# Optimization experiments

Measured on AMD Instinct MI355X. Metric: run time of the kernel, lower is better.

## Reference

```python
import jax, jax.numpy as jnp
import numpy as np
import math

B, T, M, C = 4, 2048, 16, 256   # batch, seq, m chunks, c_s chunk width
DIM = 1024                       # layer width; k = DIM // C = 4
D = 64                           # conditioning bottleneck
N_ITERS, TAU = 20, 1.0


def _diag_bias(rows, cols):
    b = np.full((rows, cols), -8.0, dtype=np.float32)
    for i in range(min(rows, cols)):
        b[i, i] = 0.0
    return jnp.asarray(b)


def setup_inputs() -> dict:
    key = jax.random.key(0)
    ks = jax.random.split(key, 10)
    state_dim = M * C
    k = DIM // C
    H_post = np.full((M, k), -8.0, dtype=np.float32)
    for i in range(M):
        H_post[i, i % k] = 0.0
    return {
        "s": jax.random.normal(ks[0], (B, T, M, C), jnp.float32),
        "gamma": 0.02 * jax.random.normal(ks[1], (state_dim,), jnp.float32),
        "compress": 0.02 * jax.random.normal(ks[2], (state_dim, D), jnp.float32),
        "alpha_pre": jnp.float32(0.01),
        "to_logits_pre": 0.02 * jax.random.normal(ks[3], (D, k * M), jnp.float32),
        "H_pre": _diag_bias(k, M),
        "alpha_align": jnp.float32(0.01),
        "to_logits_align": 0.02 * jax.random.normal(ks[4], (D, M * M), jnp.float32),
        "H_align": _diag_bias(M, M),
        "alpha_next": jnp.float32(0.01),
        "to_logits_next": 0.02 * jax.random.normal(ks[5], (D, M * M), jnp.float32),
        "H_next": _diag_bias(M, M),
        "alpha_post": jnp.float32(0.01),
        "to_logits_post": 0.02 * jax.random.normal(ks[6], (D, M * k), jnp.float32),
        "H_post": jnp.asarray(H_post),
        "W_layer": jax.random.normal(ks[7], (DIM, DIM), jnp.float32) / math.sqrt(DIM),
    }


def sinkhorn_log(logits, num_iters=N_ITERS, tau=TAU):
    """Log-domain Sinkhorn; output row-scaled so row sums = 1 * rows-normalized."""
    rows, cols = logits.shape[-2], logits.shape[-1]
    Z = logits / tau
    lr = -math.log(rows)
    lc = -math.log(cols)
    u0 = jnp.zeros(Z.shape[:-1], Z.dtype)
    v0 = jnp.zeros(Z.shape[:-2] + (cols,), Z.dtype)

    def body(_, uv):
        u, v = uv
        u = lr - jax.nn.logsumexp(Z + v[..., None, :], axis=-1)
        v = lc - jax.nn.logsumexp(Z + u[..., None], axis=-2)
        return (u, v)

    u, v = jax.lax.fori_loop(0, num_iters, body, (u0, v0))
    return jnp.exp(Z + u[..., None] + v[..., None, :]) * rows


def _route(code, alpha, to_logits, bias, state, rows, cols):
    """Fused: Sinkhorn(alpha*(code@to_logits)+bias) @ state."""
    raw = (code @ to_logits).reshape(code.shape[:-1] + (rows, cols))
    P = sinkhorn_log(alpha * raw + bias)
    return jnp.einsum('...ij,...jc->...ic', P, state)


def reference(s, gamma, compress, alpha_pre, to_logits_pre, H_pre,
              alpha_align, to_logits_align, H_align,
              alpha_next, to_logits_next, H_next,
              alpha_post, to_logits_post, H_post, W_layer):
    b, t, m, c = s.shape
    state_dim = m * c
    k = W_layer.shape[0] // c
    # RMSNorm over flattened state: F.normalize * sqrt(dim) * (gamma + 1)
    s_vec = s.reshape(b, t, state_dim)
    l2 = jnp.sqrt(jnp.sum(s_vec * s_vec, axis=-1, keepdims=True))
    s_norm = s_vec / jnp.maximum(l2, 1e-12) * jnp.sqrt(jnp.float32(state_dim)) * (gamma + 1.0)
    code = s_norm @ compress  # (b, t, d)
    # read: H_pre (k x m) routes state -> layer input
    layer_in = _route(code, alpha_pre, to_logits_pre, H_pre, s, k, m).reshape(b, t, k * c)
    layer_out = layer_in @ W_layer  # the wrapped layer_fn (dense linear)
    # write: align, absorb output via H_post, prepare next via H_next
    s_aligned = _route(code, alpha_align, to_logits_align, H_align, s, m, m)
    out_flat = layer_out.reshape(b, t, k, c)
    s_updated = s_aligned + _route(code, alpha_post, to_logits_post, H_post, out_flat, m, k)
    s_next = _route(code, alpha_next, to_logits_next, H_next, s_updated, m, m)
    return s_next
```

## Files before the change

### kernel.cpp

```cpp
#include <hip/hip_runtime.h>
#include <math.h>

#define NTOK 8192
#define SD   4096
#define ITERS 20

typedef __attribute__((ext_vector_type(8))) short short8;
typedef __attribute__((ext_vector_type(8))) unsigned short ushort8;
typedef __attribute__((ext_vector_type(4))) unsigned short us4;
typedef __attribute__((ext_vector_type(4))) float f32x4;

__device__ inline unsigned short f2bf(float x) {
    unsigned int u = __float_as_uint(x);
    unsigned int r = (u + 0x7FFFu + ((u >> 16) & 1u)) >> 16;
    return (unsigned short)r;
}
__device__ inline float bf2f(unsigned short u) {
    return __uint_as_float((unsigned int)u << 16);
}

__global__ __launch_bounds__(256) void k_prep(const float* __restrict__ compress,
                                              const float* __restrict__ gamma,
                                              unsigned short* __restrict__ cgT)
{
    __shared__ float tb[64][65];
    __shared__ float gsh[64];
    const int tid = threadIdx.x;
    const int k0 = blockIdx.x * 64;
    #pragma unroll 4
    for (int q = 0; q < 16; ++q) {
        const int idx = q * 256 + tid;
        const int r = idx >> 6, dd = idx & 63;
        tb[r][dd] = compress[(size_t)(k0 + r) * 64 + dd];
    }
    if (tid < 64) gsh[tid] = gamma[k0 + tid] + 1.0f;
    __syncthreads();
    #pragma unroll 4
    for (int q = 0; q < 16; ++q) {
        const int idx = q * 256 + tid;
        const int d = idx >> 6, r = idx & 63;
        cgT[(size_t)d * SD + k0 + r] = f2bf(tb[r][d] * gsh[r]);
    }
}

__global__ __launch_bounds__(256) void k_prept(const float* __restrict__ tl_pre,
                                               const float* __restrict__ tl_al,
                                               const float* __restrict__ tl_nx,
                                               const float* __restrict__ tl_po,
                                               unsigned short* __restrict__ tlT)
{
    const int idx = blockIdx.x * 256 + threadIdx.x;
    if (idx >= 640 * 64) return;
    const int k = idx / 640, n = idx - k * 640;
    float v;
    if (n < 64)       v = tl_pre[k * 64 + n];
    else if (n < 320) v = tl_al[k * 256 + (n - 64)];
    else if (n < 576) v = tl_nx[k * 256 + (n - 320)];
    else              v = tl_po[k * 64 + (n - 576)];
    tlT[(size_t)n * 64 + k] = f2bf(v);
}

__global__ __launch_bounds__(256) void k_wt(const float* __restrict__ W,
                                            unsigned short* __restrict__ WT)
{
    __shared__ float tb[64][65];
    const int k0 = blockIdx.y * 64, n0 = blockIdx.x * 64;
    #pragma unroll 4
    for (int q = 0; q < 16; ++q) {
        const int idx = q * 256 + threadIdx.x;
        const int r = idx >> 6, c = idx & 63;
        tb[r][c] = W[(size_t)(k0 + r) * 1024 + n0 + c];
    }
    __syncthreads();
    #pragma unroll 4
    for (int q = 0; q < 16; ++q) {
        const int idx = q * 256 + threadIdx.x;
        const int n = idx >> 6, k = idx & 63;
        WT[(size_t)(n0 + n) * 1024 + k0 + k] = f2bf(tb[k][n]);
    }
}

__global__ __launch_bounds__(256) void k_code4(const float* __restrict__ s,
                                               const unsigned short* __restrict__ cgT,
                                               unsigned short* __restrict__ codeBF,
                                               unsigned short* __restrict__ s_bf)
{
    __shared__ __align__(16) unsigned short s_sh[16 * 152];
    __shared__ __align__(16) unsigned short cg_sh[64 * 152];
    __shared__ float red[4 * 16 * 68];
    __shared__ float ssq_sh[16];
    const int tid  = threadIdx.x;
    const int lane = tid & 63;
    const int wid  = tid >> 6;
    const int tok0 = blockIdx.x * 16;
    const int st_tok = tid >> 4;
    const int st_k   = (tid & 15) * 8;
    const int sg_d   = tid >> 2;
    const int sg_k   = (tid & 3) * 32;
    const int wk = wid * 32;

    float ssq = 0.f;
    f32x4 acc[4];
    #pragma unroll
    for (int ni = 0; ni < 4; ++ni) acc[ni] = (f32x4){0.f, 0.f, 0.f, 0.f};

    for (int ks = 0; ks < 32; ++ks) {
        const int kg = ks * 128;
        __syncthreads();
        {
            const float4* sp = (const float4*)(s + (size_t)(tok0 + st_tok) * SD + kg + st_k);
            float4 v0 = sp[0], v1 = sp[1];
            ssq += v0.x*v0.x + v0.y*v0.y + v0.z*v0.z + v0.w*v0.w
                 + v1.x*v1.x + v1.y*v1.y + v1.z*v1.z + v1.w*v1.w;
            ushort8 pk;
            pk[0]=f2bf(v0.x); pk[1]=f2bf(v0.y); pk[2]=f2bf(v0.z); pk[3]=f2bf(v0.w);
            pk[4]=f2bf(v1.x); pk[5]=f2bf(v1.y); pk[6]=f2bf(v1.z); pk[7]=f2bf(v1.w);
            *(ushort8*)(s_sh + st_tok * 152 + st_k) = pk;
            if (s_bf)
                *(ushort8*)(s_bf + (size_t)(tok0 + st_tok) * SD + kg + st_k) = pk;
        }
        {
            const ushort8* gp = (const ushort8*)(cgT + (size_t)sg_d * SD + kg + sg_k);
            ushort8 c0 = gp[0], c1 = gp[1], c2 = gp[2], c3 = gp[3];
            ushort8* cw = (ushort8*)(cg_sh + sg_d * 152 + sg_k);
            cw[0] = c0; cw[1] = c1; cw[2] = c2; cw[3] = c3;
        }
        __syncthreads();

        short8 a = *(const short8*)(s_sh + (lane & 15) * 152 + wk + (lane >> 4) * 8);
        short8 b[4];
        #pragma unroll
        for (int ni = 0; ni < 4; ++ni)
            b[ni] = *(const short8*)(cg_sh + (ni * 16 + (lane & 15)) * 152 + wk + (lane >> 4) * 8);
        #pragma unroll
        for (int ni = 0; ni < 4; ++ni)
            acc[ni] = __builtin_amdgcn_mfma_f32_16x16x32_bf16(a, b[ni], acc[ni], 0, 0, 0);
    }

    ssq += __shfl_xor(ssq, 1);
    ssq += __shfl_xor(ssq, 2);
    ssq += __shfl_xor(ssq, 4);
    ssq += __shfl_xor(ssq, 8);
    if ((tid & 15) == 0) ssq_sh[st_tok] = ssq;

    #pragma unroll
    for (int ni = 0; ni < 4; ++ni)
        #pragma unroll
        for (int r = 0; r < 4; ++r)
            red[wid * 1088 + ((lane >> 4) * 4 + r) * 68 + ni * 16 + (lane & 15)] = acc[ni][r];
    __syncthreads();
    if (tid < 16) ssq_sh[tid] = 64.0f / fmaxf(sqrtf(ssq_sh[tid]), 1e-12f);
    __syncthreads();

    #pragma unroll
    for (int q = 0; q < 4; ++q) {
        const int idx = q * 256 + tid;
        const int tok = idx >> 6, d = idx & 63;
        float v = red[0 * 1088 + tok * 68 + d] + red[1 * 1088 + tok * 68 + d]
                + red[2 * 1088 + tok * 68 + d] + red[3 * 1088 + tok * 68 + d];
        codeBF[(size_t)(tok0 + tok) * 64 + d] = f2bf(v * ssq_sh[tok]);
    }
}

__global__ __launch_bounds__(256) void k_logits(const unsigned short* __restrict__ codeBF,
                                                const unsigned short* __restrict__ tlT,
                                                float* __restrict__ logits)
{
    const int tid  = threadIdx.x;
    const int lane = tid & 63;
    const int wid  = tid >> 6;
    const int m0 = blockIdx.y * 64 + wid * 16;
    const int n0 = blockIdx.x * 128;

    f32x4 acc[8];
    #pragma unroll
    for (int ni = 0; ni < 8; ++ni) acc[ni] = (f32x4){0.f, 0.f, 0.f, 0.f};

    #pragma unroll
    for (int ks = 0; ks < 2; ++ks) {
        const int ko = ks * 32 + (lane >> 4) * 8;
        short8 a = *(const short8*)(codeBF + (size_t)(m0 + (lane & 15)) * 64 + ko);
        short8 b[8];
        #pragma unroll
        for (int ni = 0; ni < 8; ++ni)
            b[ni] = *(const short8*)(tlT + (size_t)(n0 + ni * 16 + (lane & 15)) * 64 + ko);
        #pragma unroll
        for (int ni = 0; ni < 8; ++ni)
            acc[ni] = __builtin_amdgcn_mfma_f32_16x16x32_bf16(a, b[ni], acc[ni], 0, 0, 0);
    }
    #pragma unroll
    for (int ni = 0; ni < 8; ++ni)
        #pragma unroll
        for (int r = 0; r < 4; ++r)
            logits[(size_t)(m0 + (lane >> 4) * 4 + r) * 640 + n0 + ni * 16 + (lane & 15)] = acc[ni][r];
}

__global__ __launch_bounds__(256) void k_sink(const float* __restrict__ logits,
                                              const float* __restrict__ a_pre_p, const float* __restrict__ H_pre,
                                              const float* __restrict__ a_al_p,  const float* __restrict__ H_al,
                                              const float* __restrict__ a_nx_p,  const float* __restrict__ H_nx,
                                              const float* __restrict__ a_po_p,  const float* __restrict__ H_po,
                                              float* __restrict__ Ppre,
                                              float* __restrict__ Pna, float* __restrict__ Pnp)
{
    __shared__ float Pal_sh[16 * 260];
    __shared__ float Pnx_sh[16 * 260];
    __shared__ float Ppo_sh[16 * 68];
    const int tid  = threadIdx.x;
    const int lane = tid & 63;
    const int wid  = tid >> 6;
    const int tok0 = blockIdx.x * 16;
    const int t_in = lane >> 2;
    const int sub  = lane & 3;
    const int tok  = tok0 + t_in;

    if (wid < 2) {
        const float alpha = (wid == 0) ? (*a_al_p) : (*a_nx_p);
        const float* Hp   = ((wid == 0) ? H_al : H_nx) + sub * 64;
        const float* lgp  = logits + (size_t)tok * 640 + (wid == 0 ? 64 : 320) + sub * 64;
        float Km[4][16];
        #pragma unroll
        for (int rr = 0; rr < 4; ++rr)
            #pragma unroll
            for (int c4 = 0; c4 < 4; ++c4) {
                float4 rv = *(const float4*)(lgp + rr * 16 + c4 * 4);
                float4 hv = *(const float4*)(Hp  + rr * 16 + c4 * 4);
                Km[rr][c4*4+0] = expf(alpha * rv.x + hv.x);
                Km[rr][c4*4+1] = expf(alpha * rv.y + hv.y);
                Km[rr][c4*4+2] = expf(alpha * rv.z + hv.z);
                Km[rr][c4*4+3] = expf(alpha * rv.w + hv.w);
            }
        float v[16], u[4];
        #pragma unroll
        for (int c = 0; c < 16; ++c) v[c] = 1.0f;
        for (int it = 0; it < ITERS; ++it) {
            #pragma unroll
            for (int rr = 0; rr < 4; ++rr) {
                float su = 0.f;
                #pragma unroll
                for (int c = 0; c < 16; ++c) su += Km[rr][c] * v[c];
                u[rr] = 0.0625f * __builtin_amdgcn_rcpf(su);
            }
            float pv[16];
            #pragma unroll
            for (int c = 0; c < 16; ++c)
                pv[c] = Km[0][c]*u[0] + Km[1][c]*u[1] + Km[2][c]*u[2] + Km[3][c]*u[3];
            #pragma unroll
            for (int c = 0; c < 16; ++c) pv[c] += __shfl_xor(pv[c], 1);
            #pragma unroll
            for (int c = 0; c < 16; ++c) pv[c] += __shfl_xor(pv[c], 2);
            #pragma unroll
            for (int c = 0; c < 16; ++c) v[c] = 0.0625f * __builtin_amdgcn_rcpf(pv[c]);
        }
        float* dst = ((wid == 0) ? Pal_sh : Pnx_sh) + t_in * 260;
        #pragma unroll
        for (int rr = 0; rr < 4; ++rr) {
            const float su16 = 16.0f * u[rr];
            #pragma unroll
            for (int c = 0; c < 16; ++c)
                dst[(sub * 4 + rr) * 16 + c] = Km[rr][c] * su16 * v[c];
        }
    } else if (wid == 2) {
        const float alpha = *a_pre_p;
        const float* lgp = logits + (size_t)tok * 640 + sub * 16;
        const float* Hp  = H_pre + sub * 16;
        float Km[16];
        #pragma unroll
        for (int c4 = 0; c4 < 4; ++c4) {
            float4 rv = *(const float4*)(lgp + c4 * 4);
            float4 hv = *(const float4*)(Hp  + c4 * 4);
            Km[c4*4+0] = expf(alpha * rv.x + hv.x);
            Km[c4*4+1] = expf(alpha * rv.y + hv.y);
            Km[c4*4+2] = expf(alpha * rv.z + hv.z);
            Km[c4*4+3] = expf(alpha * rv.w + hv.w);
        }
        float v[16], u;
        #pragma unroll
        for (int c = 0; c < 16; ++c) v[c] = 1.0f;
        for (int it = 0; it < ITERS; ++it) {
            float su = 0.f;
            #pragma unroll
            for (int c = 0; c < 16; ++c) su += Km[c] * v[c];
            u = 0.25f * __builtin_amdgcn_rcpf(su);
            float pv[16];
            #pragma unroll
            for (int c = 0; c < 16; ++c) pv[c] = Km[c] * u;
            #pragma unroll
            for (int c = 0; c < 16; ++c) pv[c] += __shfl_xor(pv[c], 1);
            #pragma unroll
            for (int c = 0; c < 16; ++c) pv[c] += __shfl_xor(pv[c], 2);
            #pragma unroll
            for (int c = 0; c < 16; ++c) v[c] = 0.0625f * __builtin_amdgcn_rcpf(pv[c]);
        }
        const float su4 = 4.0f * u;
        #pragma unroll
        for (int c = 0; c < 16; ++c)
            Ppre[(size_t)tok * 64 + sub * 16 + c] = Km[c] * su4 * v[c];
    } else {
        const float alpha = *a_po_p;
        const float* lgp = logits + (size_t)tok * 640 + 576 + sub * 16;
        const float* Hp  = H_po + sub * 16;
        float Km[4][4];
        #pragma unroll
        for (int rr = 0; rr < 4; ++rr) {
            float4 rv = *(const float4*)(lgp + rr * 4);
            float4 hv = *(const float4*)(Hp  + rr * 4);
            Km[rr][0] = expf(alpha * rv.x + hv.x);
            Km[rr][1] = expf(alpha * rv.y + hv.y);
            Km[rr][2] = expf(alpha * rv.z + hv.z);
            Km[rr][3] = expf(alpha * rv.w + hv.w);
        }
        float v[4], u[4];
        #pragma unroll
        for (int c = 0; c < 4; ++c) v[c] = 1.0f;
        for (int it = 0; it < ITERS; ++it) {
            #pragma unroll
            for (int rr = 0; rr < 4; ++rr) {
                float su = 0.f;
                #pragma unroll
                for (int c = 0; c < 4; ++c) su += Km[rr][c] * v[c];
                u[rr] = 0.0625f * __builtin_amdgcn_rcpf(su);
            }
            float pv[4];
            #pragma unroll
            for (int c = 0; c < 4; ++c)
                pv[c] = Km[0][c]*u[0] + Km[1][c]*u[1] + Km[2][c]*u[2] + Km[3][c]*u[3];
            #pragma unroll
            for (int c = 0; c < 4; ++c) pv[c] += __shfl_xor(pv[c], 1);
            #pragma unroll
            for (int c = 0; c < 4; ++c) pv[c] += __shfl_xor(pv[c], 2);
            #pragma unroll
            for (int c = 0; c < 4; ++c) v[c] = 0.25f * __builtin_amdgcn_rcpf(pv[c]);
        }
        #pragma unroll
        for (int rr = 0; rr < 4; ++rr) {
            const float su16 = 16.0f * u[rr];
            #pragma unroll
            for (int c = 0; c < 4; ++c)
                Ppo_sh[t_in * 68 + (sub * 4 + rr) * 4 + c] = Km[rr][c] * su16 * v[c];
        }
    }
    __syncthreads();

    const int ct = tid >> 4;
    const int cj = tid & 15;
    const float* pnx = Pnx_sh + ct * 260;
    const float* pal = Pal_sh + ct * 260;
    const float* ppo = Ppo_sh + ct * 68;
    #pragma unroll
    for (int m = 0; m < 16; ++m) {
        float acc = 0.f;
        #pragma unroll
        for (int t2 = 0; t2 < 16; ++t2) acc += pnx[m * 16 + t2] * pal[t2 * 16 + cj];
        Pna[(size_t)(tok0 + ct) * 256 + m * 16 + cj] = acc;
    }
    #pragma unroll
    for (int e = 0; e < 4; ++e) {
        const int idx = cj * 4 + e;
        const int m = idx >> 2, q = idx & 3;
        float acc = 0.f;
        #pragma unroll
        for (int t2 = 0; t2 < 16; ++t2) acc += pnx[m * 16 + t2] * ppo[t2 * 4 + q];
        Pnp[(size_t)(tok0 + ct) * 64 + idx] = acc;
    }
}

template<bool SBF>
__global__ __launch_bounds__(256) void k_apply2(const float* __restrict__ s,
                                                const unsigned short* __restrict__ s_bf,
                                                const float* __restrict__ Ppre,
                                                unsigned short* __restrict__ layer_in)
{
    __shared__ float s_sh[SD];
    __shared__ float P_sh[64];
    const int tid = threadIdx.x;
    const int tok = blockIdx.x;

    if (SBF) {
        #pragma unroll
        for (int c2 = 0; c2 < 2; ++c2) {
            ushort8 v = *(const ushort8*)(s_bf + (size_t)tok * SD + c2 * 2048 + tid * 8);
            float4 f0, f1;
            f0.x = bf2f(v[0]); f0.y = bf2f(v[1]); f0.z = bf2f(v[2]); f0.w = bf2f(v[3]);
            f1.x = bf2f(v[4]); f1.y = bf2f(v[5]); f1.z = bf2f(v[6]); f1.w = bf2f(v[7]);
            *(float4*)(s_sh + c2 * 2048 + tid * 8)     = f0;
            *(float4*)(s_sh + c2 * 2048 + tid * 8 + 4) = f1;
        }
    } else {
        const float4* sp4 = (const float4*)(s + (size_t)tok * SD);
        #pragma unroll
        for (int j = 0; j < 4; ++j)
            *(float4*)(s_sh + j * 1024 + tid * 4) = sp4[j * 256 + tid];
    }
    if (tid < 64) P_sh[tid] = Ppre[(size_t)tok * 64 + tid];
    __syncthreads();

    #pragma unroll
    for (int i = 0; i < 4; ++i) {
        float acc = 0.f;
        #pragma unroll
        for (int j = 0; j < 16; ++j) acc += P_sh[i * 16 + j] * s_sh[j * 256 + tid];
        layer_in[(size_t)tok * 1024 + i * 256 + tid] = f2bf(acc);
    }
}

__global__ __launch_bounds__(256) void k_gemm_bf16(const unsigned short* __restrict__ A,
                                                   const unsigned short* __restrict__ BT,
                                                   unsigned short* __restrict__ Cb)
{
    __shared__ unsigned short Abuf[128 * 48];
    __shared__ unsigned short Bbuf[128 * 48];
    const int tid  = threadIdx.x;
    const int lane = tid & 63;
    const int wid  = tid >> 6;
    const int wr   = wid >> 1, wc = wid & 1;
    const int m0 = blockIdx.y * 128, n0 = blockIdx.x * 128;

    f32x4 acc[4][4];
    #pragma unroll
    for (int mi = 0; mi < 4; ++mi)
        #pragma unroll
        for (int ni = 0; ni < 4; ++ni) acc[mi][ni] = (f32x4){0.f, 0.f, 0.f, 0.f};

    for (int k0 = 0; k0 < 1024; k0 += 32) {
        __syncthreads();
        #pragma unroll
        for (int h = 0; h < 2; ++h) {
            const int idx = h * 256 + tid;
            const int row = idx >> 2, kq = idx & 3;
            float4 av = *(const float4*)(A + (size_t)(m0 + row) * 1024 + k0 + kq * 8);
            *(float4*)(Abuf + row * 48 + kq * 8) = av;
            float4 bv = *(const float4*)(BT + (size_t)(n0 + row) * 1024 + k0 + kq * 8);
            *(float4*)(Bbuf + row * 48 + kq * 8) = bv;
        }
        __syncthreads();

        short8 a[4], b[4];
        #pragma unroll
        for (int mi = 0; mi < 4; ++mi)
            a[mi] = *(const short8*)(Abuf + (wr * 64 + mi * 16 + (lane & 15)) * 48 + (lane >> 4) * 8);
        #pragma unroll
        for (int ni = 0; ni < 4; ++ni)
            b[ni] = *(const short8*)(Bbuf + (wc * 64 + ni * 16 + (lane & 15)) * 48 + (lane >> 4) * 8);
        #pragma unroll
        for (int mi = 0; mi < 4; ++mi)
            #pragma unroll
            for (int ni = 0; ni < 4; ++ni)
                acc[mi][ni] = __builtin_amdgcn_mfma_f32_16x16x32_bf16(a[mi], b[ni], acc[mi][ni], 0, 0, 0);
    }

    #pragma unroll
    for (int mi = 0; mi < 4; ++mi)
        #pragma unroll
        for (int ni = 0; ni < 4; ++ni)
            #pragma unroll
            for (int r = 0; r < 4; ++r)
                Cb[(size_t)(m0 + wr * 64 + mi * 16 + (lane >> 4) * 4 + r) * 1024 +
                   n0 + wc * 64 + ni * 16 + (lane & 15)] = f2bf(acc[mi][ni][r]);
}

template<bool SBF>
__global__ __launch_bounds__(256) void k_final2(const float* __restrict__ s,
                                                const unsigned short* __restrict__ s_bf,
                                                const unsigned short* __restrict__ lo_bf,
                                                const float* __restrict__ Pna,
                                                const float* __restrict__ Pnp,
                                                float* __restrict__ out)
{
    __shared__ float s_sh[SD];
    __shared__ float lo_sh[1024];
    __shared__ float Pna_sh[256];
    __shared__ float Pnp_sh[64];
    const int tid = threadIdx.x;
    const int tok = blockIdx.x;

    if (SBF) {
        #pragma unroll
        for (int c2 = 0; c2 < 2; ++c2) {
            ushort8 v = *(const ushort8*)(s_bf + (size_t)tok * SD + c2 * 2048 + tid * 8);
            float4 f0, f1;
            f0.x = bf2f(v[0]); f0.y = bf2f(v[1]); f0.z = bf2f(v[2]); f0.w = bf2f(v[3]);
            f1.x = bf2f(v[4]); f1.y = bf2f(v[5]); f1.z = bf2f(v[6]); f1.w = bf2f(v[7]);
            *(float4*)(s_sh + c2 * 2048 + tid * 8)     = f0;
            *(float4*)(s_sh + c2 * 2048 + tid * 8 + 4) = f1;
        }
    } else {
        const float4* sp4 = (const float4*)(s + (size_t)tok * SD);
        #pragma unroll
        for (int j = 0; j < 4; ++j)
            *(float4*)(s_sh + j * 1024 + tid * 4) = sp4[j * 256 + tid];
    }
    {
        us4 lv = *(const us4*)(lo_bf + (size_t)tok * 1024 + tid * 4);
        float4 f;
        f.x = bf2f(lv[0]); f.y = bf2f(lv[1]); f.z = bf2f(lv[2]); f.w = bf2f(lv[3]);
        *(float4*)(lo_sh + tid * 4) = f;
    }
    Pna_sh[tid] = Pna[(size_t)tok * 256 + tid];
    if (tid < 64) Pnp_sh[tid] = Pnp[(size_t)tok * 64 + tid];
    __syncthreads();

    const int c = tid;
    #pragma unroll
    for (int m = 0; m < 16; ++m) {
        float acc = 0.f;
        #pragma unroll
        for (int j = 0; j < 16; ++j) acc += Pna_sh[m * 16 + j] * s_sh[j * 256 + c];
        #pragma unroll
        for (int q = 0; q < 4; ++q) acc += Pnp_sh[m * 4 + q] * lo_sh[q * 256 + c];
        out[(size_t)tok * SD + m * 256 + c] = acc;
    }
}

extern "C" void kernel_launch(void* const* d_in, const int* in_sizes, int n_in,
                              void* d_out, int out_size, void* d_ws, size_t ws_size,
                              hipStream_t stream)
{
    const float* s        = (const float*)d_in[0];
    const float* gamma    = (const float*)d_in[1];
    const float* compress = (const float*)d_in[2];
    const float* a_pre    = (const float*)d_in[3];
    const float* tl_pre   = (const float*)d_in[4];
    const float* H_pre    = (const float*)d_in[5];
    const float* a_al     = (const float*)d_in[6];
    const float* tl_al    = (const float*)d_in[7];
    const float* H_al     = (const float*)d_in[8];
    const float* a_nx     = (const float*)d_in[9];
    const float* tl_nx    = (const float*)d_in[10];
    const float* H_nx     = (const float*)d_in[11];
    const float* a_po     = (const float*)d_in[12];
    const float* tl_po    = (const float*)d_in[13];
    const float* H_po     = (const float*)d_in[14];
    const float* W        = (const float*)d_in[15];
    float* out = (float*)d_out;

    char* p = (char*)d_ws;
    float* layer_out         = (float*)p;          p += (size_t)8192 * 1024 * 4;
    float* logits            = layer_out;
    unsigned short* lo_bf    = (unsigned short*)layer_out;
    float* Pna               = (float*)p;          p += (size_t)8192 * 256 * 4;
    float* Pnp               = (float*)p;          p += (size_t)8192 * 64 * 4;
    unsigned short* layer_in = (unsigned short*)p; p += (size_t)8192 * 1024 * 2;
    unsigned short* WT       = (unsigned short*)p; p += (size_t)1024 * 1024 * 2;
    unsigned short* cgT      = (unsigned short*)p; p += (size_t)64 * SD * 2;
    unsigned short* codeBF   = (unsigned short*)p; p += (size_t)8192 * 64 * 2;
    unsigned short* tlT      = (unsigned short*)p; p += (size_t)640 * 64 * 2 + 128;
    float* Ppre              = (float*)p;          p += (size_t)8192 * 64 * 4;
    unsigned short* s_bf     = (unsigned short*)p; p += (size_t)NTOK * SD * 2;
    const bool use_sbf = ((size_t)(p - (char*)d_ws) <= ws_size);

    k_wt<<<dim3(16, 16), 256, 0, stream>>>(W, WT);
    k_prep<<<64, 256, 0, stream>>>(compress, gamma, cgT);
    k_prept<<<160, 256, 0, stream>>>(tl_pre, tl_al, tl_nx, tl_po, tlT);
    k_code4<<<512, 256, 0, stream>>>(s, cgT, codeBF, use_sbf ? s_bf : (unsigned short*)nullptr);
    k_logits<<<dim3(5, 128), 256, 0, stream>>>(codeBF, tlT, logits);
    k_sink<<<512, 256, 0, stream>>>(logits,
                                    a_pre, H_pre, a_al, H_al,
                                    a_nx, H_nx, a_po, H_po,
                                    Ppre, Pna, Pnp);
    if (use_sbf) {
        k_apply2<true><<<NTOK, 256, 0, stream>>>(s, s_bf, Ppre, layer_in);
    } else {
        k_apply2<false><<<NTOK, 256, 0, stream>>>(s, s_bf, Ppre, layer_in);
    }
    k_gemm_bf16<<<dim3(8, 64), 256, 0, stream>>>(layer_in, WT, lo_bf);
    if (use_sbf) {
        k_final2<true><<<NTOK, 256, 0, stream>>>(s, s_bf, lo_bf, Pna, Pnp, out);
    } else {
        k_final2<false><<<NTOK, 256, 0, stream>>>(s, s_bf, lo_bf, Pna, Pnp, out);
    }
}
```

Measured before the change: 214.5 us.

## Fuse code projection, logits GEMM and Sinkhorn into one front kernel

Merges the three weight-prep kernels into a single launch and fuses the compress projection, the logits MFMA and the Sinkhorn routing into one per-16-token kernel. Code vectors and logits now stay in shared memory (logits stored as bf16) instead of going through global memory. This removes four launches and the logits round trip, at the cost of about 64KB of LDS per block, which lowers occupancy, and slightly reduced logits precision.

```diff
diff --git a/kernel.cpp b/kernel.cpp
--- a/kernel.cpp
+++ b/kernel.cpp
@@ -19,76 +19,83 @@
     return __uint_as_float((unsigned int)u << 16);
 }
 
-__global__ __launch_bounds__(256) void k_prep(const float* __restrict__ compress,
-                                              const float* __restrict__ gamma,
-                                              unsigned short* __restrict__ cgT)
+__global__ __launch_bounds__(256) void k_preall(const float* __restrict__ W, unsigned short* __restrict__ WT,
+                                                const float* __restrict__ compress, const float* __restrict__ gamma,
+                                                unsigned short* __restrict__ cgT,
+                                                const float* __restrict__ tl_pre, const float* __restrict__ tl_al,
+                                                const float* __restrict__ tl_nx,  const float* __restrict__ tl_po,
+                                                unsigned short* __restrict__ tlT)
 {
-    __shared__ float tb[64][65];
-    __shared__ float gsh[64];
+    const int b = blockIdx.x;
     const int tid = threadIdx.x;
-    const int k0 = blockIdx.x * 64;
-    #pragma unroll 4
-    for (int q = 0; q < 16; ++q) {
-        const int idx = q * 256 + tid;
-        const int r = idx >> 6, dd = idx & 63;
-        tb[r][dd] = compress[(size_t)(k0 + r) * 64 + dd];
-    }
-    if (tid < 64) gsh[tid] = gamma[k0 + tid] + 1.0f;
-    __syncthreads();
-    #pragma unroll 4
-    for (int q = 0; q < 16; ++q) {
-        const int idx = q * 256 + tid;
-        const int d = idx >> 6, r = idx & 63;
-        cgT[(size_t)d * SD + k0 + r] = f2bf(tb[r][d] * gsh[r]);
-    }
-}
-
-__global__ __launch_bounds__(256) void k_prept(const float* __restrict__ tl_pre,
-                                               const float* __restrict__ tl_al,
-                                               const float* __restrict__ tl_nx,
-                                               const float* __restrict__ tl_po,
-                                               unsigned short* __restrict__ tlT)
-{
-    const int idx = blockIdx.x * 256 + threadIdx.x;
-    if (idx >= 640 * 64) return;
-    const int k = idx / 640, n = idx - k * 640;
-    float v;
-    if (n < 64)       v = tl_pre[k * 64 + n];
-    else if (n < 320) v = tl_al[k * 256 + (n - 64)];
-    else if (n < 576) v = tl_nx[k * 256 + (n - 320)];
-    else              v = tl_po[k * 64 + (n - 576)];
-    tlT[(size_t)n * 64 + k] = f2bf(v);
-}
-
-__global__ __launch_bounds__(256) void k_wt(const float* __restrict__ W,
-                                            unsigned short* __restrict__ WT)
-{
-    __shared__ float tb[64][65];
-    const int k0 = blockIdx.y * 64, n0 = blockIdx.x * 64;
-    #pragma unroll 4
-    for (int q = 0; q < 16; ++q) {
-        const int idx = q * 256 + threadIdx.x;
-        const int r = idx >> 6, c = idx & 63;
-        tb[r][c] = W[(size_t)(k0 + r) * 1024 + n0 + c];
-    }
-    __syncthreads();
-    #pragma unroll 4
-    for (int q = 0; q < 16; ++q) {
-        const int idx = q * 256 + threadIdx.x;
-        const int n = idx >> 6, k = idx & 63;
-        WT[(size_t)(n0 + n) * 1024 + k0 + k] = f2bf(tb[k][n]);
-    }
-}
-
-__global__ __launch_bounds__(256) void k_code4(const float* __restrict__ s,
+    if (b < 256) {
+        __shared__ float tb[64][65];
+        const int k0 = (b >> 4) * 64, n0 = (b & 15) * 64;
+        #pragma unroll 4
+        for (int q = 0; q < 16; ++q) {
+            const int idx = q * 256 + tid;
+            const int r = idx >> 6, c = idx & 63;
+            tb[r][c] = W[(size_t)(k0 + r) * 1024 + n0 + c];
+        }
+        __syncthreads();
+        #pragma unroll 4
+        for (int q = 0; q < 16; ++q) {
+            const int idx = q * 256 + tid;
+            const int n = idx >> 6, k = idx & 63;
+            WT[(size_t)(n0 + n) * 1024 + k0 + k] = f2bf(tb[k][n]);
+        }
+    } else if (b < 320) {
+        __shared__ float tb2[64][65];
+        __shared__ float gsh[64];
+        const int k0 = (b - 256) * 64;
+        #pragma unroll 4
+        for (int q = 0; q < 16; ++q) {
+            const int idx = q * 256 + tid;
+            const int r = idx >> 6, dd = idx & 63;
+            tb2[r][dd] = compress[(size_t)(k0 + r) * 64 + dd];
+        }
+        if (tid < 64) gsh[tid] = gamma[k0 + tid] + 1.0f;
+        __syncthreads();
+        #pragma unroll 4
+        for (int q = 0; q < 16; ++q) {
+            const int idx = q * 256 + tid;
+            const int d = idx >> 6, r = idx & 63;
+            cgT[(size_t)d * SD + k0 + r] = f2bf(tb2[r][d] * gsh[r]);
+        }
+    } else {
+        const int idx = (b - 320) * 256 + tid;
+        const int k = idx / 640, n = idx - k * 640;
+        float v;
+        if (n < 64)       v = tl_pre[k * 64 + n];
+        else if (n < 320) v = tl_al[k * 256 + (n - 64)];
+        else if (n < 576) v = tl_nx[k * 256 + (n - 320)];
+        else              v = tl_po[k * 64 + (n - 576)];
+        tlT[(size_t)n * 64 + k] = f2bf(v);
+    }
+}
+
+__global__ __launch_bounds__(256) void k_front(const float* __restrict__ s,
                                                const unsigned short* __restrict__ cgT,
-                                               unsigned short* __restrict__ codeBF,
+                                               const unsigned short* __restrict__ tlT,
+                                               const float* __restrict__ a_pre_p, const float* __restrict__ H_pre,
+                                               const float* __restrict__ a_al_p,  const float* __restrict__ H_al,
+                                               const float* __restrict__ a_nx_p,  const float* __restrict__ H_nx,
+                                               const float* __restrict__ a_po_p,  const float* __restrict__ H_po,
+                                               float* __restrict__ Ppre,
+                                               float* __restrict__ Pna, float* __restrict__ Pnp,
                                                unsigned short* __restrict__ s_bf)
 {
-    __shared__ __align__(16) unsigned short s_sh[16 * 152];
-    __shared__ __align__(16) unsigned short cg_sh[64 * 152];
-    __shared__ float red[4 * 16 * 68];
-    __shared__ float ssq_sh[16];
+    __shared__ __align__(16) char smem[64320];
+    unsigned short* code_sh = (unsigned short*)(smem);
+    unsigned short* s_sh    = (unsigned short*)(smem + 2304);
+    unsigned short* cg_sh   = (unsigned short*)(smem + 2304 + 4864);
+    float*          red     = (float*)(smem + 2304);
+    unsigned short* lg_sh   = (unsigned short*)(smem + 2304);
+    float*          Pal_sh  = (float*)(smem + 26624);
+    float*          Pnx_sh  = (float*)(smem + 43264);
+    float*          Ppo_sh  = (float*)(smem + 59904);
+    float*          ssq_sh  = (float*)(smem + 64256);
+
     const int tid  = threadIdx.x;
     const int lane = tid & 63;
     const int wid  = tid >> 6;
@@ -141,6 +148,7 @@
     ssq += __shfl_xor(ssq, 2);
     ssq += __shfl_xor(ssq, 4);
     ssq += __shfl_xor(ssq, 8);
+    __syncthreads();
     if ((tid & 15) == 0) ssq_sh[st_tok] = ssq;
 
     #pragma unroll
@@ -151,65 +159,39 @@
     __syncthreads();
     if (tid < 16) ssq_sh[tid] = 64.0f / fmaxf(sqrtf(ssq_sh[tid]), 1e-12f);
     __syncthreads();
-
     #pragma unroll
     for (int q = 0; q < 4; ++q) {
         const int idx = q * 256 + tid;
         const int tok = idx >> 6, d = idx & 63;
         float v = red[0 * 1088 + tok * 68 + d] + red[1 * 1088 + tok * 68 + d]
                 + red[2 * 1088 + tok * 68 + d] + red[3 * 1088 + tok * 68 + d];
-        codeBF[(size_t)(tok0 + tok) * 64 + d] = f2bf(v * ssq_sh[tok]);
-    }
-}
-
-__global__ __launch_bounds__(256) void k_logits(const unsigned short* __restrict__ codeBF,
-                                                const unsigned short* __restrict__ tlT,
-                                                float* __restrict__ logits)
-{
-    const int tid  = threadIdx.x;
-    const int lane = tid & 63;
-    const int wid  = tid >> 6;
-    const int m0 = blockIdx.y * 64 + wid * 16;
-    const int n0 = blockIdx.x * 128;
-
-    f32x4 acc[8];
-    #pragma unroll
-    for (int ni = 0; ni < 8; ++ni) acc[ni] = (f32x4){0.f, 0.f, 0.f, 0.f};
-
-    #pragma unroll
-    for (int ks = 0; ks < 2; ++ks) {
-        const int ko = ks * 32 + (lane >> 4) * 8;
-        short8 a = *(const short8*)(codeBF + (size_t)(m0 + (lane & 15)) * 64 + ko);
-        short8 b[8];
-        #pragma unroll
-        for (int ni = 0; ni < 8; ++ni)
-            b[ni] = *(const short8*)(tlT + (size_t)(n0 + ni * 16 + (lane & 15)) * 64 + ko);
-        #pragma unroll
-        for (int ni = 0; ni < 8; ++ni)
-            acc[ni] = __builtin_amdgcn_mfma_f32_16x16x32_bf16(a, b[ni], acc[ni], 0, 0, 0);
-    }
-    #pragma unroll
-    for (int ni = 0; ni < 8; ++ni)
-        #pragma unroll
-        for (int r = 0; r < 4; ++r)
-            logits[(size_t)(m0 + (lane >> 4) * 4 + r) * 640 + n0 + ni * 16 + (lane & 15)] = acc[ni][r];
-}
-
-__global__ __launch_bounds__(256) void k_sink(const float* __restrict__ logits,
-                                              const float* __restrict__ a_pre_p, const float* __restrict__ H_pre,
-                                              const float* __restrict__ a_al_p,  const float* __restrict__ H_al,
-                                              const float* __restrict__ a_nx_p,  const float* __restrict__ H_nx,
-                                              const float* __restrict__ a_po_p,  const float* __restrict__ H_po,
-                                              float* __restrict__ Ppre,
-                                              float* __restrict__ Pna, float* __restrict__ Pnp)
-{
-    __shared__ float Pal_sh[16 * 260];
-    __shared__ float Pnx_sh[16 * 260];
-    __shared__ float Ppo_sh[16 * 68];
-    const int tid  = threadIdx.x;
-    const int lane = tid & 63;
-    const int wid  = tid >> 6;
-    const int tok0 = blockIdx.x * 16;
+        code_sh[tok * 72 + d] = f2bf(v * ssq_sh[tok]);
+    }
+    __syncthreads();
+
+    {
+        f32x4 acc2[10];
+        #pragma unroll
+        for (int ni = 0; ni < 10; ++ni) acc2[ni] = (f32x4){0.f, 0.f, 0.f, 0.f};
+        const int nbase = wid * 160;
+        #pragma unroll
+        for (int ks = 0; ks < 2; ++ks) {
+            const int ko = ks * 32 + (lane >> 4) * 8;
+            short8 a = *(const short8*)(code_sh + (lane & 15) * 72 + ko);
+            #pragma unroll
+            for (int ni = 0; ni < 10; ++ni) {
+                short8 b = *(const short8*)(tlT + (size_t)(nbase + ni * 16 + (lane & 15)) * 64 + ko);
+                acc2[ni] = __builtin_amdgcn_mfma_f32_16x16x32_bf16(a, b, acc2[ni], 0, 0, 0);
+            }
+        }
+        #pragma unroll
+        for (int ni = 0; ni < 10; ++ni)
+            #pragma unroll
+            for (int r = 0; r < 4; ++r)
+                lg_sh[((lane >> 4) * 4 + r) * 656 + nbase + ni * 16 + (lane & 15)] = f2bf(acc2[ni][r]);
+    }
+    __syncthreads();
+
     const int t_in = lane >> 2;
     const int sub  = lane & 3;
     const int tok  = tok0 + t_in;
@@ -217,18 +199,23 @@
     if (wid < 2) {
         const float alpha = (wid == 0) ? (*a_al_p) : (*a_nx_p);
         const float* Hp   = ((wid == 0) ? H_al : H_nx) + sub * 64;
-        const float* lgp  = logits + (size_t)tok * 640 + (wid == 0 ? 64 : 320) + sub * 64;
+        const unsigned short* lgp = lg_sh + t_in * 656 + (wid == 0 ? 64 : 320) + sub * 64;
         float Km[4][16];
         #pragma unroll
         for (int rr = 0; rr < 4; ++rr)
             #pragma unroll
-            for (int c4 = 0; c4 < 4; ++c4) {
-                float4 rv = *(const float4*)(lgp + rr * 16 + c4 * 4);
-                float4 hv = *(const float4*)(Hp  + rr * 16 + c4 * 4);
-                Km[rr][c4*4+0] = expf(alpha * rv.x + hv.x);
-                Km[rr][c4*4+1] = expf(alpha * rv.y + hv.y);
-                Km[rr][c4*4+2] = expf(alpha * rv.z + hv.z);
-                Km[rr][c4*4+3] = expf(alpha * rv.w + hv.w);
+            for (int h = 0; h < 2; ++h) {
+                ushort8 rv = *(const ushort8*)(lgp + rr * 16 + h * 8);
+                float4 h0 = *(const float4*)(Hp + rr * 16 + h * 8);
+                float4 h1 = *(const float4*)(Hp + rr * 16 + h * 8 + 4);
+                Km[rr][h*8+0] = expf(alpha * bf2f(rv[0]) + h0.x);
+                Km[rr][h*8+1] = expf(alpha * bf2f(rv[1]) + h0.y);
+                Km[rr][h*8+2] = expf(alpha * bf2f(rv[2]) + h0.z);
+                Km[rr][h*8+3] = expf(alpha * bf2f(rv[3]) + h0.w);
+                Km[rr][h*8+4] = expf(alpha * bf2f(rv[4]) + h1.x);
+                Km[rr][h*8+5] = expf(alpha * bf2f(rv[5]) + h1.y);
+                Km[rr][h*8+6] = expf(alpha * bf2f(rv[6]) + h1.z);
+                Km[rr][h*8+7] = expf(alpha * bf2f(rv[7]) + h1.w);
             }
         float v[16], u[4];
         #pragma unroll
@@ -262,17 +249,22 @@
         }
     } else if (wid == 2) {
         const float alpha = *a_pre_p;
-        const float* lgp = logits + (size_t)tok * 640 + sub * 16;
+        const unsigned short* lgp = lg_sh + t_in * 656 + sub * 16;
         const float* Hp  = H_pre + sub * 16;
         float Km[16];
         #pragma unroll
-        for (int c4 = 0; c4 < 4; ++c4) {
-            float4 rv = *(const float4*)(lgp + c4 * 4);
-            float4 hv = *(const float4*)(Hp  + c4 * 4);
-            Km[c4*4+0] = expf(alpha * rv.x + hv.x);
-            Km[c4*4+1] = expf(alpha * rv.y + hv.y);
-            Km[c4*4+2] = expf(alpha * rv.z + hv.z);
-            Km[c4*4+3] = expf(alpha * rv.w + hv.w);
+        for (int h = 0; h < 2; ++h) {
+            ushort8 rv = *(const ushort8*)(lgp + h * 8);
+            float4 h0 = *(const float4*)(Hp + h * 8);
+            float4 h1 = *(const float4*)(Hp + h * 8 + 4);
+            Km[h*8+0] = expf(alpha * bf2f(rv[0]) + h0.x);
+            Km[h*8+1] = expf(alpha * bf2f(rv[1]) + h0.y);
+            Km[h*8+2] = expf(alpha * bf2f(rv[2]) + h0.z);
+            Km[h*8+3] = expf(alpha * bf2f(rv[3]) + h0.w);
+            Km[h*8+4] = expf(alpha * bf2f(rv[4]) + h1.x);
+            Km[h*8+5] = expf(alpha * bf2f(rv[5]) + h1.y);
+            Km[h*8+6] = expf(alpha * bf2f(rv[6]) + h1.z);
+            Km[h*8+7] = expf(alpha * bf2f(rv[7]) + h1.w);
         }
         float v[16], u;
         #pragma unroll
@@ -298,17 +290,17 @@
             Ppre[(size_t)tok * 64 + sub * 16 + c] = Km[c] * su4 * v[c];
     } else {
         const float alpha = *a_po_p;
-        const float* lgp = logits + (size_t)tok * 640 + 576 + sub * 16;
+        const unsigned short* lgp = lg_sh + t_in * 656 + 576 + sub * 16;
         const float* Hp  = H_po + sub * 16;
         float Km[4][4];
         #pragma unroll
         for (int rr = 0; rr < 4; ++rr) {
-            float4 rv = *(const float4*)(lgp + rr * 4);
-            float4 hv = *(const float4*)(Hp  + rr * 4);
-            Km[rr][0] = expf(alpha * rv.x + hv.x);
-            Km[rr][1] = expf(alpha * rv.y + hv.y);
-            Km[rr][2] = expf(alpha * rv.z + hv.z);
-            Km[rr][3] = expf(alpha * rv.w + hv.w);
+            us4 rv = *(const us4*)(lgp + rr * 4);
+            float4 hv = *(const float4*)(Hp + rr * 4);
+            Km[rr][0] = expf(alpha * bf2f(rv[0]) + hv.x);
+            Km[rr][1] = expf(alpha * bf2f(rv[1]) + hv.y);
+            Km[rr][2] = expf(alpha * bf2f(rv[2]) + hv.z);
+            Km[rr][3] = expf(alpha * bf2f(rv[3]) + hv.w);
         }
         float v[4], u[4];
         #pragma unroll
@@ -349,19 +341,19 @@
     const float* ppo = Ppo_sh + ct * 68;
     #pragma unroll
     for (int m = 0; m < 16; ++m) {
-        float acc = 0.f;
-        #pragma unroll
-        for (int t2 = 0; t2 < 16; ++t2) acc += pnx[m * 16 + t2] * pal[t2 * 16 + cj];
-        Pna[(size_t)(tok0 + ct) * 256 + m * 16 + cj] = acc;
+        float a2 = 0.f;
+        #pragma unroll
+        for (int t2 = 0; t2 < 16; ++t2) a2 += pnx[m * 16 + t2] * pal[t2 * 16 + cj];
+        Pna[(size_t)(tok0 + ct) * 256 + m * 16 + cj] = a2;
     }
     #pragma unroll
     for (int e = 0; e < 4; ++e) {
         const int idx = cj * 4 + e;
         const int m = idx >> 2, q = idx & 3;
-        float acc = 0.f;
-        #pragma unroll
-        for (int t2 = 0; t2 < 16; ++t2) acc += pnx[m * 16 + t2] * ppo[t2 * 4 + q];
-        Pnp[(size_t)(tok0 + ct) * 64 + idx] = acc;
+        float a2 = 0.f;
+        #pragma unroll
+        for (int t2 = 0; t2 < 16; ++t2) a2 += pnx[m * 16 + t2] * ppo[t2 * 4 + q];
+        Pnp[(size_t)(tok0 + ct) * 64 + idx] = a2;
     }
 }
 
@@ -535,29 +527,24 @@
     float* out = (float*)d_out;
 
     char* p = (char*)d_ws;
-    float* layer_out         = (float*)p;          p += (size_t)8192 * 1024 * 4;
-    float* logits            = layer_out;
-    unsigned short* lo_bf    = (unsigned short*)layer_out;
+    unsigned short* lo_bf    = (unsigned short*)p; p += (size_t)8192 * 1024 * 2;
     float* Pna               = (float*)p;          p += (size_t)8192 * 256 * 4;
     float* Pnp               = (float*)p;          p += (size_t)8192 * 64 * 4;
     unsigned short* layer_in = (unsigned short*)p; p += (size_t)8192 * 1024 * 2;
     unsigned short* WT       = (unsigned short*)p; p += (size_t)1024 * 1024 * 2;
     unsigned short* cgT      = (unsigned short*)p; p += (size_t)64 * SD * 2;
-    unsigned short* codeBF   = (unsigned short*)p; p += (size_t)8192 * 64 * 2;
     unsigned short* tlT      = (unsigned short*)p; p += (size_t)640 * 64 * 2 + 128;
     float* Ppre              = (float*)p;          p += (size_t)8192 * 64 * 4;
     unsigned short* s_bf     = (unsigned short*)p; p += (size_t)NTOK * SD * 2;
     const bool use_sbf = ((size_t)(p - (char*)d_ws) <= ws_size);
 
-    k_wt<<<dim3(16, 16), 256, 0, stream>>>(W, WT);
-    k_prep<<<64, 256, 0, stream>>>(compress, gamma, cgT);
-    k_prept<<<160, 256, 0, stream>>>(tl_pre, tl_al, tl_nx, tl_po, tlT);
-    k_code4<<<512, 256, 0, stream>>>(s, cgT, codeBF, use_sbf ? s_bf : (unsigned short*)nullptr);
-    k_logits<<<dim3(5, 128), 256, 0, stream>>>(codeBF, tlT, logits);
-    k_sink<<<512, 256, 0, stream>>>(logits,
-                                    a_pre, H_pre, a_al, H_al,
-                                    a_nx, H_nx, a_po, H_po,
-                                    Ppre, Pna, Pnp);
+    k_preall<<<480, 256, 0, stream>>>(W, WT, compress, gamma, cgT,
+                                      tl_pre, tl_al, tl_nx, tl_po, tlT);
+    k_front<<<512, 256, 0, stream>>>(s, cgT, tlT,
+                                     a_pre, H_pre, a_al, H_al,
+                                     a_nx, H_nx, a_po, H_po,
+                                     Ppre, Pna, Pnp,
+                                     use_sbf ? s_bf : (unsigned short*)nullptr);
     if (use_sbf) {
         k_apply2<true><<<NTOK, 256, 0, stream>>>(s, s_bf, Ppre, layer_in);
     } else {
```

Result: faster. 195.9 us (-8.7%).
